# Performance work log

Hardware: AMD Instinct MI355X
Metric: run time of the kernel (lower is better)

Reference implementation:

```python
import jax, jax.numpy as jnp
import numpy as np
import math

B, S, E, H = 2, 2048, 64, 8
N_LAYER = 12
EPS = 1e-5


def setup_inputs() -> dict:
    key = jax.random.key(0)
    ks = jax.random.split(key, 7)
    x = jax.random.normal(ks[0], (B, S, E), dtype=jnp.float32)
    ln_w = jnp.ones((E,), dtype=jnp.float32)
    W_q = 0.02 * jax.random.normal(ks[1], (H, E, E), dtype=jnp.float32)
    W_k = 0.02 * jax.random.normal(ks[2], (H, E, E), dtype=jnp.float32)
    W_v = 0.02 * jax.random.normal(ks[3], (H, E, E), dtype=jnp.float32)
    W_o = (0.02 / math.sqrt(2 * N_LAYER)) * jax.random.normal(ks[4], (E, H * E), dtype=jnp.float32)
    gamma = 1.0 + 0.02 * jax.random.normal(ks[5], (H, 1, 1), dtype=jnp.float32)
    return {"x": x, "ln_w": ln_w, "W_q": W_q, "W_k": W_k, "W_v": W_v, "W_o": W_o, "gamma": gamma}


def reference(x, ln_w, W_q, W_k, W_v, W_o, gamma):
    # LayerNorm (bias=False)
    mu = jnp.mean(x, axis=-1, keepdims=True)
    var = jnp.mean((x - mu) ** 2, axis=-1, keepdims=True)
    xn = (x - mu) * jax.lax.rsqrt(var + EPS) * ln_w  # [B,S,E]

    # per-head full-rank projections: x repeated across heads
    Q = jnp.einsum('bse,hef->bhsf', xn, W_q)  # [B,H,S,E]
    K = jnp.einsum('bse,hef->bhsf', xn, W_k)
    V = jnp.einsum('bse,hef->bhsf', xn, W_v)

    # RBF attention scores: exp(-gamma * ||q_i - k_j||^2 / sqrt(E)), causal
    q2 = jnp.sum(Q * Q, axis=-1)[..., :, None]          # [B,H,S,1]
    k2 = jnp.sum(K * K, axis=-1)[..., None, :]          # [B,H,1,S]
    qk = jnp.einsum('bhse,bhte->bhst', Q, K)            # [B,H,S,S]
    sqdist = q2 + k2 - 2.0 * qk
    scores = jnp.exp(-gamma[None] * sqdist / math.sqrt(E))  # gamma broadcast [H,1,1]
    causal = jnp.tril(jnp.ones((S, S), dtype=scores.dtype))
    scores = scores * causal

    out = jnp.einsum('bhst,bhte->bhse', scores, V)       # [B,H,S,E]
    out = out.transpose(0, 2, 1, 3).reshape(B, S, H * E)  # concat heads
    out = out @ W_o.T                                     # [B,S,E]
    return out
```

## Files before the change

kernel.cpp:

```cpp
#include <hip/hip_runtime.h>
#include <math.h>

typedef __attribute__((ext_vector_type(8))) short bf8;
typedef __attribute__((ext_vector_type(4))) short s4v;
typedef __attribute__((ext_vector_type(16))) float f16v;
typedef __attribute__((ext_vector_type(4))) float f4v;
typedef __attribute__((ext_vector_type(4))) int i4v;

constexpr int CS = 2048;
constexpr float EPS = 1e-5f;
constexpr float LOG2E = 1.44269504088896f;

static __device__ inline short f2bf(float x) {
  union { float f; unsigned u; } v; v.f = x;
  unsigned r = (v.u + 0x7FFFu + ((v.u >> 16) & 1u)) >> 16;
  return (short)r;
}
static __device__ inline float bf2f(short u) {
  union { unsigned u; float f; } v;
  v.u = ((unsigned)(unsigned short)u) << 16;
  return v.f;
}
static __device__ inline unsigned cvt_pk_bf16(float lo, float hi) {
  unsigned d;
  asm("v_cvt_pk_bf16_f32 %0, %1, %2" : "=v"(d) : "v"(lo), "v"(hi));
  return d;
}

__global__ __launch_bounds__(256) void k_qkv(const float* __restrict__ x, const float* __restrict__ ln_w,
                                             const float* __restrict__ Wq, const float* __restrict__ Wk,
                                             const float* __restrict__ Wv, const float* __restrict__ gamma,
                                             short* __restrict__ Qf, short* __restrict__ Kf,
                                             short* __restrict__ Vf, float* __restrict__ aqg) {
  __shared__ short WtL[3 * 64 * 72];
  __shared__ short QtL[2 * 32 * 72];
  __shared__ short KtL[2 * 32 * 72];
  __shared__ float q2s[64];
  __shared__ float bks[64];
  int blk = blockIdx.x;
  int bh = blk & 15, st = blk >> 4;
  int b = bh >> 3, h = bh & 7;
  int t = threadIdx.x, wid = t >> 6, lane = t & 63;
  int l31 = lane & 31, g = lane >> 5;
  int sh = wid >> 1, fh = wid & 1;
  int f = fh * 32 + l31;

  {
    int e0 = (t >> 4) * 4, f0 = (t & 15) * 4;
    const float* srcs[3];
    srcs[0] = Wq + h * 4096; srcs[1] = Wk + h * 4096; srcs[2] = Wv + h * 4096;
#pragma unroll
    for (int wsel = 0; wsel < 3; ++wsel) {
      const float* src = srcs[wsel];
      f4v r0 = *(const f4v*)&src[(e0 + 0) * 64 + f0];
      f4v r1 = *(const f4v*)&src[(e0 + 1) * 64 + f0];
      f4v r2 = *(const f4v*)&src[(e0 + 2) * 64 + f0];
      f4v r3 = *(const f4v*)&src[(e0 + 3) * 64 + f0];
      short* dst = &WtL[wsel * 4608];
      s4v c0, c1, c2, c3;
      c0[0] = f2bf(r0.x); c0[1] = f2bf(r1.x); c0[2] = f2bf(r2.x); c0[3] = f2bf(r3.x);
      c1[0] = f2bf(r0.y); c1[1] = f2bf(r1.y); c1[2] = f2bf(r2.y); c1[3] = f2bf(r3.y);
      c2[0] = f2bf(r0.z); c2[1] = f2bf(r1.z); c2[2] = f2bf(r2.z); c2[3] = f2bf(r3.z);
      c3[0] = f2bf(r0.w); c3[1] = f2bf(r1.w); c3[2] = f2bf(r2.w); c3[3] = f2bf(r3.w);
      *(s4v*)&dst[(f0 + 0) * 72 + e0] = c0;
      *(s4v*)&dst[(f0 + 1) * 72 + e0] = c1;
      *(s4v*)&dst[(f0 + 2) * 72 + e0] = c2;
      *(s4v*)&dst[(f0 + 3) * 72 + e0] = c3;
    }
  }

  int row = b * CS + st * 64 + sh * 32 + l31;
  f4v xv[8];
#pragma unroll
  for (int ks = 0; ks < 4; ++ks) {
    xv[2 * ks]     = *(const f4v*)&x[row * 64 + ks * 16 + g * 8];
    xv[2 * ks + 1] = *(const f4v*)&x[row * 64 + ks * 16 + g * 8 + 4];
  }
  float s = 0.f;
#pragma unroll
  for (int m = 0; m < 8; ++m) s += xv[m].x + xv[m].y + xv[m].z + xv[m].w;
  s += __shfl_xor(s, 32, 64);
  float mu = s * (1.f / 64.f);
  float vs = 0.f;
#pragma unroll
  for (int m = 0; m < 8; ++m) {
#pragma unroll
    for (int j = 0; j < 4; ++j) { float d = xv[m][j] - mu; vs += d * d; }
  }
  vs += __shfl_xor(vs, 32, 64);
  float rs = rsqrtf(vs * (1.f / 64.f) + EPS);
  bf8 af[4];
#pragma unroll
  for (int ks = 0; ks < 4; ++ks) {
    f4v lw0 = *(const f4v*)&ln_w[ks * 16 + g * 8];
    f4v lw1 = *(const f4v*)&ln_w[ks * 16 + g * 8 + 4];
#pragma unroll
    for (int j = 0; j < 4; ++j) {
      af[ks][j]     = f2bf((xv[2 * ks][j] - mu) * rs * lw0[j]);
      af[ks][j + 4] = f2bf((xv[2 * ks + 1][j] - mu) * rs * lw1[j]);
    }
  }
  float gh = gamma[h];
  float cgk = -gh * 0.125f * LOG2E;
  float cgq = gh * 0.25f * LOG2E;
  float icgq2 = 1.f / (cgq * cgq);
  __syncthreads();

  f16v cq; for (int i = 0; i < 16; ++i) cq[i] = 0.f;
#pragma unroll
  for (int ks = 0; ks < 4; ++ks) {
    bf8 bw = *(const bf8*)&WtL[0 * 4608 + f * 72 + ks * 16 + g * 8];
    cq = __builtin_amdgcn_mfma_f32_32x32x16_bf16(af[ks], bw, cq, 0, 0, 0);
  }
#pragma unroll
  for (int r = 0; r < 16; ++r) {
    int rl = (r & 3) + 8 * (r >> 2) + 4 * g;
    QtL[(sh * 32 + rl) * 72 + f] = f2bf(cq[r] * cgq);
  }
  f16v ck; for (int i = 0; i < 16; ++i) ck[i] = 0.f;
#pragma unroll
  for (int ks = 0; ks < 4; ++ks) {
    bf8 bw = *(const bf8*)&WtL[1 * 4608 + f * 72 + ks * 16 + g * 8];
    ck = __builtin_amdgcn_mfma_f32_32x32x16_bf16(af[ks], bw, ck, 0, 0, 0);
  }
#pragma unroll
  for (int r = 0; r < 16; ++r) {
    int rl = (r & 3) + 8 * (r >> 2) + 4 * g;
    KtL[(sh * 32 + rl) * 72 + f] = f2bf(ck[r]);
  }
  f16v cv; for (int i = 0; i < 16; ++i) cv[i] = 0.f;
#pragma unroll
  for (int ks = 0; ks < 4; ++ks) {
    bf8 bw = *(const bf8*)&WtL[2 * 4608 + f * 72 + ks * 16 + g * 8];
    cv = __builtin_amdgcn_mfma_f32_32x32x16_bf16(af[ks], bw, cv, 0, 0, 0);
  }
  __syncthreads();

  {
    int rw = t >> 2, q4 = t & 3;
    float sq = 0.f, sk = 0.f;
#pragma unroll
    for (int m = 0; m < 2; ++m) {
      bf8 vq = *(bf8*)&QtL[rw * 72 + q4 * 16 + m * 8];
      bf8 vk = *(bf8*)&KtL[rw * 72 + q4 * 16 + m * 8];
#pragma unroll
      for (int j = 0; j < 8; ++j) {
        float xq = bf2f(vq[j]); sq += xq * xq;
        float xk = bf2f(vk[j]); sk += xk * xk;
      }
    }
    sq += __shfl_xor(sq, 1, 64); sq += __shfl_xor(sq, 2, 64);
    sk += __shfl_xor(sk, 1, 64); sk += __shfl_xor(sk, 2, 64);
    if (q4 == 0) {
      q2s[rw] = sq * icgq2;
      bks[rw] = exp2f(cgk * sk);
    }
  }
  {
    int ktloc = t >> 7, lm = (t >> 1) & 63, jh = t & 1;
#pragma unroll
    for (int ks = 0; ks < 4; ++ks) {
      int laddr = (ktloc * 32 + (lm & 31)) * 72 + ks * 16 + (lm >> 5) * 8 + jh * 4;
      int gaddr = ((bh * 64 + st * 2 + ktloc) * 4 + ks) * 512 + lm * 8 + jh * 4;
      *(s4v*)&Qf[gaddr] = *(s4v*)&QtL[laddr];
      *(s4v*)&Kf[gaddr] = *(s4v*)&KtL[laddr];
    }
  }
  __syncthreads();

  int kt = st * 2 + sh;
#pragma unroll
  for (int m = 0; m < 4; ++m) {
    s4v pk;
#pragma unroll
    for (int c = 0; c < 4; ++c) {
      int rl = sh * 32 + c + 8 * m + 4 * g;
      pk[c] = f2bf(cv[m * 4 + c] * bks[rl]);
    }
    int addr = ((((bh * 64 + kt) * 2 + fh) * 2 + (m >> 1)) * 64 + (m & 1) * 32 + l31) * 8 + 4 * g;
    *(s4v*)&Vf[addr] = pk;
  }
  if (t < 64) {
    aqg[bh * CS + st * 64 + t] = exp2f(cgk * q2s[t]);
  }
}

__global__ __launch_bounds__(512, 4) void k_attn(const short* __restrict__ Qf, const short* __restrict__ Kf,
                                                 const short* __restrict__ Vf, const float* __restrict__ aqg,
                                                 const float* __restrict__ gamma, short* __restrict__ attnB) {
  __shared__ float red4[4][64][37];
  int bid = blockIdx.x;
  int bh = ((bid & 7) << 1) | ((bid >> 3) & 1);
  int qt = 63 - (bid >> 4);
  int b = bh >> 3, h = bh & 7;
  int t = threadIdx.x, w = t >> 6, lane = t & 63;
  int lam = lane & 31, g = lane >> 5;
  int L = qt + 1;
  int lo = (w * L) >> 3, hi = ((w + 1) * L) >> 3;
  int hiND = hi < qt ? hi : qt;

  bf8 qf[4];
#pragma unroll
  for (int ks = 0; ks < 4; ++ks) qf[ks] = *(const bf8*)&Qf[((bh * 64 + qt) * 4 + ks) * 512 + lane * 8];

  f16v oa0, oa1;
#pragma unroll
  for (int rr = 0; rr < 16; ++rr) { oa0[rr] = 0.f; oa1[rr] = 0.f; }

  const short* kfb = Kf + bh * 131072 + lane * 8;
  const short* vfb = Vf + bh * 131072 + lane * 8;

  for (int kt = lo; kt < hiND; ++kt) {
    const short* kp = kfb + kt * 2048;
    bf8 ak0 = *(const bf8*)(kp);
    bf8 ak1 = *(const bf8*)(kp + 512);
    bf8 ak2 = *(const bf8*)(kp + 1024);
    bf8 ak3 = *(const bf8*)(kp + 1536);

    f16v ct;
#pragma unroll
    for (int rr = 0; rr < 16; ++rr) ct[rr] = 0.f;
    __builtin_amdgcn_s_setprio(1);
    ct = __builtin_amdgcn_mfma_f32_32x32x16_bf16(ak0, qf[0], ct, 0, 0, 0);
    ct = __builtin_amdgcn_mfma_f32_32x32x16_bf16(ak1, qf[1], ct, 0, 0, 0);
    ct = __builtin_amdgcn_mfma_f32_32x32x16_bf16(ak2, qf[2], ct, 0, 0, 0);
    ct = __builtin_amdgcn_mfma_f32_32x32x16_bf16(ak3, qf[3], ct, 0, 0, 0);
    __builtin_amdgcn_s_setprio(0);

    const short* vp = vfb + kt * 2048;
    bf8 av00 = *(const bf8*)(vp);
    bf8 av01 = *(const bf8*)(vp + 512);
    bf8 av10 = *(const bf8*)(vp + 1024);
    bf8 av11 = *(const bf8*)(vp + 1536);

    unsigned pkA[4], pkB[4];
#pragma unroll
    for (int m = 0; m < 4; ++m) {
      float e0 = exp2f(ct[4 * m + 0]);
      float e1 = exp2f(ct[4 * m + 1]);
      float e2 = exp2f(ct[4 * m + 2]);
      float e3 = exp2f(ct[4 * m + 3]);
      pkA[m] = cvt_pk_bf16(e0, e1);
      pkB[m] = cvt_pk_bf16(e2, e3);
    }
    __builtin_amdgcn_s_setprio(1);
#pragma unroll
    for (int ks2 = 0; ks2 < 2; ++ks2) {
      unsigned a0 = pkA[2 * ks2], a1 = pkA[2 * ks2 + 1];
      unsigned b0 = pkB[2 * ks2], b1 = pkB[2 * ks2 + 1];
      asm("v_permlane32_swap_b32 %0, %1" : "+v"(a0), "+v"(a1));
      asm("v_permlane32_swap_b32 %0, %1" : "+v"(b0), "+v"(b1));
      i4v wv;
      wv.x = (int)a0; wv.y = (int)b0; wv.z = (int)a1; wv.w = (int)b1;
      bf8 bs = *(bf8*)&wv;
      oa0 = __builtin_amdgcn_mfma_f32_32x32x16_bf16(ks2 ? av01 : av00, bs, oa0, 0, 0, 0);
      oa1 = __builtin_amdgcn_mfma_f32_32x32x16_bf16(ks2 ? av11 : av10, bs, oa1, 0, 0, 0);
    }
    __builtin_amdgcn_s_setprio(0);
  }

  if (hi > hiND) {
    int kt = qt;
    const short* kp = kfb + kt * 2048;
    bf8 ak0 = *(const bf8*)(kp);
    bf8 ak1 = *(const bf8*)(kp + 512);
    bf8 ak2 = *(const bf8*)(kp + 1024);
    bf8 ak3 = *(const bf8*)(kp + 1536);

    f16v ct;
#pragma unroll
    for (int rr = 0; rr < 16; ++rr) ct[rr] = 0.f;
    ct = __builtin_amdgcn_mfma_f32_32x32x16_bf16(ak0, qf[0], ct, 0, 0, 0);
    ct = __builtin_amdgcn_mfma_f32_32x32x16_bf16(ak1, qf[1], ct, 0, 0, 0);
    ct = __builtin_amdgcn_mfma_f32_32x32x16_bf16(ak2, qf[2], ct, 0, 0, 0);
    ct = __builtin_amdgcn_mfma_f32_32x32x16_bf16(ak3, qf[3], ct, 0, 0, 0);

    const short* vp = vfb + kt * 2048;
    bf8 av00 = *(const bf8*)(vp);
    bf8 av01 = *(const bf8*)(vp + 512);
    bf8 av10 = *(const bf8*)(vp + 1024);
    bf8 av11 = *(const bf8*)(vp + 1536);

    unsigned pkA[4], pkB[4];
#pragma unroll
    for (int m = 0; m < 4; ++m) {
      float sv[4];
#pragma unroll
      for (int ii = 0; ii < 4; ++ii) {
        int kloc = ii + 8 * m + 4 * g;
        float ev = exp2f(ct[4 * m + ii]);
        if (kloc > lam) ev = 0.f;
        sv[ii] = ev;
      }
      pkA[m] = cvt_pk_bf16(sv[0], sv[1]);
      pkB[m] = cvt_pk_bf16(sv[2], sv[3]);
    }
#pragma unroll
    for (int ks2 = 0; ks2 < 2; ++ks2) {
      unsigned a0 = pkA[2 * ks2], a1 = pkA[2 * ks2 + 1];
      unsigned b0 = pkB[2 * ks2], b1 = pkB[2 * ks2 + 1];
      asm("v_permlane32_swap_b32 %0, %1" : "+v"(a0), "+v"(a1));
      asm("v_permlane32_swap_b32 %0, %1" : "+v"(b0), "+v"(b1));
      i4v wv;
      wv.x = (int)a0; wv.y = (int)b0; wv.z = (int)a1; wv.w = (int)b1;
      bf8 bs = *(bf8*)&wv;
      oa0 = __builtin_amdgcn_mfma_f32_32x32x16_bf16(ks2 ? av01 : av00, bs, oa0, 0, 0, 0);
      oa1 = __builtin_amdgcn_mfma_f32_32x32x16_bf16(ks2 ? av11 : av10, bs, oa1, 0, 0, 0);
    }
  }

  if (w < 4) {
#pragma unroll
    for (int rr = 0; rr < 16; ++rr) {
      int e = (rr & 3) + 8 * (rr >> 2) + 4 * g;
      red4[w][e][lam] = oa0[rr];
      red4[w][e + 32][lam] = oa1[rr];
    }
  }
  __syncthreads();
  if (w >= 4) {
#pragma unroll
    for (int rr = 0; rr < 16; ++rr) {
      int e = (rr & 3) + 8 * (rr >> 2) + 4 * g;
      red4[w - 4][e][lam] += oa0[rr];
      red4[w - 4][e + 32][lam] += oa1[rr];
    }
  }
  __syncthreads();
  {
    int q = t >> 4, e0 = (t & 15) * 4;
    float aqv = aqg[bh * CS + qt * 32 + q];
    s4v ov;
#pragma unroll
    for (int jj = 0; jj < 4; ++jj) {
      float v = red4[0][e0 + jj][q] + red4[1][e0 + jj][q] + red4[2][e0 + jj][q] + red4[3][e0 + jj][q];
      ov[jj] = f2bf(v * aqv);
    }
    *(s4v*)&attnB[(b * CS + qt * 32 + q) * 512 + h * 64 + e0] = ov;
  }
}

__global__ __launch_bounds__(256) void k_proj(const short* __restrict__ attnB, const float* __restrict__ Wo,
                                              float* __restrict__ out) {
  __shared__ float red[4][32][36];
  int blk = blockIdx.x, t = threadIdx.x;
  int rt = blk >> 1, fh2 = blk & 1;
  int r0 = rt * 32;
  int kw = t >> 6, lane = t & 63, l31 = lane & 31, g = lane >> 5;
  f16v c; for (int i = 0; i < 16; ++i) c[i] = 0.f;
  int arow = (r0 + l31) * 512;
  int fw = fh2 * 32 + l31;
#pragma unroll
  for (int ks = 0; ks < 8; ++ks) {
    int k0 = kw * 128 + ks * 16 + g * 8;
    bf8 a = *(const bf8*)&attnB[arow + k0];
    f4v w0 = *(const f4v*)&Wo[fw * 512 + k0];
    f4v w1 = *(const f4v*)&Wo[fw * 512 + k0 + 4];
    i4v wp;
    wp.x = (int)cvt_pk_bf16(w0.x, w0.y);
    wp.y = (int)cvt_pk_bf16(w0.z, w0.w);
    wp.z = (int)cvt_pk_bf16(w1.x, w1.y);
    wp.w = (int)cvt_pk_bf16(w1.z, w1.w);
    bf8 bw = *(bf8*)&wp;
    c = __builtin_amdgcn_mfma_f32_32x32x16_bf16(a, bw, c, 0, 0, 0);
  }
#pragma unroll
  for (int rr = 0; rr < 16; ++rr) {
    int rw = (rr & 3) + 8 * (rr >> 2) + 4 * g;
    red[kw][rw][l31] = c[rr];
  }
  __syncthreads();
  {
    int rw = t >> 3, f4 = (t & 7) * 4;
    f4v sum;
#pragma unroll
    for (int j = 0; j < 4; ++j)
      sum[j] = red[0][rw][f4 + j] + red[1][rw][f4 + j] + red[2][rw][f4 + j] + red[3][rw][f4 + j];
    *(f4v*)&out[(r0 + rw) * 64 + fh2 * 32 + f4] = sum;
  }
}

extern "C" void kernel_launch(void* const* d_in, const int* in_sizes, int n_in,
                              void* d_out, int out_size, void* d_ws, size_t ws_size,
                              hipStream_t stream) {
  const float* x     = (const float*)d_in[0];
  const float* ln_w  = (const float*)d_in[1];
  const float* Wq    = (const float*)d_in[2];
  const float* Wk    = (const float*)d_in[3];
  const float* Wv    = (const float*)d_in[4];
  const float* Wo    = (const float*)d_in[5];
  const float* gamma = (const float*)d_in[6];
  float* out = (float*)d_out;

  char* w = (char*)d_ws;
  short* Qf    = (short*)w;
  short* Kf    = (short*)(w + 4194304);
  short* Vf    = (short*)(w + 2 * 4194304);
  float* aqg   = (float*)(w + 3 * 4194304);
  short* attnB = (short*)(w + 3 * 4194304 + 131072);

  hipLaunchKernelGGL(k_qkv,  dim3(512),  dim3(256), 0, stream, x, ln_w, Wq, Wk, Wv, gamma, Qf, Kf, Vf, aqg);
  hipLaunchKernelGGL(k_attn, dim3(1024), dim3(512), 0, stream, Qf, Kf, Vf, aqg, gamma, attnB);
  hipLaunchKernelGGL(k_proj, dim3(256),  dim3(256), 0, stream, attnB, Wo, out);
}
```

Measured before the change: 41.12 us.

## Split attention key range across two blocks and sum partials in projection

Each query tile's causal key range is now split in half across two 256-thread blocks, giving twice as many smaller blocks. Query tiles are interleaved short/long to balance the load. Each half writes its own bf16 partial output buffer, and the output projection runs an extra MFMA per step to add the two partials. Q fragments now come from shared memory instead of registers, which frees registers for higher occupancy. The cost is extra partial-buffer traffic, double bf16 rounding, and more A-operand loads in the projection kernel.

```diff
diff --git a/kernel.cpp b/kernel.cpp
--- a/kernel.cpp
+++ b/kernel.cpp
@@ -185,30 +185,39 @@
   }
 }
 
-__global__ __launch_bounds__(512, 4) void k_attn(const short* __restrict__ Qf, const short* __restrict__ Kf,
+__global__ __launch_bounds__(256, 5) void k_attn(const short* __restrict__ Qf, const short* __restrict__ Kf,
                                                  const short* __restrict__ Vf, const float* __restrict__ aqg,
-                                                 const float* __restrict__ gamma, short* __restrict__ attnB) {
-  __shared__ float red4[4][64][37];
+                                                 const float* __restrict__ gamma,
+                                                 short* __restrict__ P0, short* __restrict__ P1) {
+  __shared__ short QsL[2048];
+  __shared__ float red2[2][64][33];
   int bid = blockIdx.x;
   int bh = ((bid & 7) << 1) | ((bid >> 3) & 1);
-  int qt = 63 - (bid >> 4);
+  int half = (bid >> 4) & 1;
+  int z = bid >> 5;
+  int y = z & 7, j = z >> 3, m = j >> 1;
+  int qt = (j & 1) ? (4 * y + m) : (63 - (4 * y + m));
   int b = bh >> 3, h = bh & 7;
   int t = threadIdx.x, w = t >> 6, lane = t & 63;
   int lam = lane & 31, g = lane >> 5;
   int L = qt + 1;
-  int lo = (w * L) >> 3, hi = ((w + 1) * L) >> 3;
+  int kmid = (qt + 2) >> 1;
+  int k0 = half ? kmid : 0;
+  int k1 = half ? L : kmid;
+  int R = k1 - k0;
+  int lo = k0 + ((w * R) >> 2), hi = k0 + (((w + 1) * R) >> 2);
   int hiND = hi < qt ? hi : qt;
-
-  bf8 qf[4];
-#pragma unroll
-  for (int ks = 0; ks < 4; ++ks) qf[ks] = *(const bf8*)&Qf[((bh * 64 + qt) * 4 + ks) * 512 + lane * 8];
-
+  bool ownDiag = (qt >= lo) && (qt < hi);
+
+  *(bf8*)&QsL[t * 8] = *(const bf8*)&Qf[(bh * 64 + qt) * 2048 + t * 8];
   f16v oa0, oa1;
 #pragma unroll
   for (int rr = 0; rr < 16; ++rr) { oa0[rr] = 0.f; oa1[rr] = 0.f; }
+  __syncthreads();
 
   const short* kfb = Kf + bh * 131072 + lane * 8;
   const short* vfb = Vf + bh * 131072 + lane * 8;
+  int qidx = lane * 8;
 
   for (int kt = lo; kt < hiND; ++kt) {
     const short* kp = kfb + kt * 2048;
@@ -217,14 +226,20 @@
     bf8 ak2 = *(const bf8*)(kp + 1024);
     bf8 ak3 = *(const bf8*)(kp + 1536);
 
+    asm volatile("" : "+v"(qidx));
+    bf8 q0 = *(bf8*)&QsL[qidx];
+    bf8 q1 = *(bf8*)&QsL[qidx + 512];
+    bf8 q2 = *(bf8*)&QsL[qidx + 1024];
+    bf8 q3 = *(bf8*)&QsL[qidx + 1536];
+
     f16v ct;
 #pragma unroll
     for (int rr = 0; rr < 16; ++rr) ct[rr] = 0.f;
     __builtin_amdgcn_s_setprio(1);
-    ct = __builtin_amdgcn_mfma_f32_32x32x16_bf16(ak0, qf[0], ct, 0, 0, 0);
-    ct = __builtin_amdgcn_mfma_f32_32x32x16_bf16(ak1, qf[1], ct, 0, 0, 0);
-    ct = __builtin_amdgcn_mfma_f32_32x32x16_bf16(ak2, qf[2], ct, 0, 0, 0);
-    ct = __builtin_amdgcn_mfma_f32_32x32x16_bf16(ak3, qf[3], ct, 0, 0, 0);
+    ct = __builtin_amdgcn_mfma_f32_32x32x16_bf16(ak0, q0, ct, 0, 0, 0);
+    ct = __builtin_amdgcn_mfma_f32_32x32x16_bf16(ak1, q1, ct, 0, 0, 0);
+    ct = __builtin_amdgcn_mfma_f32_32x32x16_bf16(ak2, q2, ct, 0, 0, 0);
+    ct = __builtin_amdgcn_mfma_f32_32x32x16_bf16(ak3, q3, ct, 0, 0, 0);
     __builtin_amdgcn_s_setprio(0);
 
     const short* vp = vfb + kt * 2048;
@@ -235,13 +250,13 @@
 
     unsigned pkA[4], pkB[4];
 #pragma unroll
-    for (int m = 0; m < 4; ++m) {
-      float e0 = exp2f(ct[4 * m + 0]);
-      float e1 = exp2f(ct[4 * m + 1]);
-      float e2 = exp2f(ct[4 * m + 2]);
-      float e3 = exp2f(ct[4 * m + 3]);
-      pkA[m] = cvt_pk_bf16(e0, e1);
-      pkB[m] = cvt_pk_bf16(e2, e3);
+    for (int mm = 0; mm < 4; ++mm) {
+      float e0 = exp2f(ct[4 * mm + 0]);
+      float e1 = exp2f(ct[4 * mm + 1]);
+      float e2 = exp2f(ct[4 * mm + 2]);
+      float e3 = exp2f(ct[4 * mm + 3]);
+      pkA[mm] = cvt_pk_bf16(e0, e1);
+      pkB[mm] = cvt_pk_bf16(e2, e3);
     }
     __builtin_amdgcn_s_setprio(1);
 #pragma unroll
@@ -259,21 +274,25 @@
     __builtin_amdgcn_s_setprio(0);
   }
 
-  if (hi > hiND) {
+  if (ownDiag) {
     int kt = qt;
     const short* kp = kfb + kt * 2048;
     bf8 ak0 = *(const bf8*)(kp);
     bf8 ak1 = *(const bf8*)(kp + 512);
     bf8 ak2 = *(const bf8*)(kp + 1024);
     bf8 ak3 = *(const bf8*)(kp + 1536);
+    bf8 q0 = *(bf8*)&QsL[qidx];
+    bf8 q1 = *(bf8*)&QsL[qidx + 512];
+    bf8 q2 = *(bf8*)&QsL[qidx + 1024];
+    bf8 q3 = *(bf8*)&QsL[qidx + 1536];
 
     f16v ct;
 #pragma unroll
     for (int rr = 0; rr < 16; ++rr) ct[rr] = 0.f;
-    ct = __builtin_amdgcn_mfma_f32_32x32x16_bf16(ak0, qf[0], ct, 0, 0, 0);
-    ct = __builtin_amdgcn_mfma_f32_32x32x16_bf16(ak1, qf[1], ct, 0, 0, 0);
-    ct = __builtin_amdgcn_mfma_f32_32x32x16_bf16(ak2, qf[2], ct, 0, 0, 0);
-    ct = __builtin_amdgcn_mfma_f32_32x32x16_bf16(ak3, qf[3], ct, 0, 0, 0);
+    ct = __builtin_amdgcn_mfma_f32_32x32x16_bf16(ak0, q0, ct, 0, 0, 0);
+    ct = __builtin_amdgcn_mfma_f32_32x32x16_bf16(ak1, q1, ct, 0, 0, 0);
+    ct = __builtin_amdgcn_mfma_f32_32x32x16_bf16(ak2, q2, ct, 0, 0, 0);
+    ct = __builtin_amdgcn_mfma_f32_32x32x16_bf16(ak3, q3, ct, 0, 0, 0);
 
     const short* vp = vfb + kt * 2048;
     bf8 av00 = *(const bf8*)(vp);
@@ -283,17 +302,17 @@
 
     unsigned pkA[4], pkB[4];
 #pragma unroll
-    for (int m = 0; m < 4; ++m) {
+    for (int mm = 0; mm < 4; ++mm) {
       float sv[4];
 #pragma unroll
       for (int ii = 0; ii < 4; ++ii) {
-        int kloc = ii + 8 * m + 4 * g;
-        float ev = exp2f(ct[4 * m + ii]);
+        int kloc = ii + 8 * mm + 4 * g;
+        float ev = exp2f(ct[4 * mm + ii]);
         if (kloc > lam) ev = 0.f;
         sv[ii] = ev;
       }
-      pkA[m] = cvt_pk_bf16(sv[0], sv[1]);
-      pkB[m] = cvt_pk_bf16(sv[2], sv[3]);
+      pkA[mm] = cvt_pk_bf16(sv[0], sv[1]);
+      pkB[mm] = cvt_pk_bf16(sv[2], sv[3]);
     }
 #pragma unroll
     for (int ks2 = 0; ks2 < 2; ++ks2) {
@@ -309,51 +328,54 @@
     }
   }
 
-  if (w < 4) {
+  if (w < 2) {
 #pragma unroll
     for (int rr = 0; rr < 16; ++rr) {
       int e = (rr & 3) + 8 * (rr >> 2) + 4 * g;
-      red4[w][e][lam] = oa0[rr];
-      red4[w][e + 32][lam] = oa1[rr];
-    }
-  }
-  __syncthreads();
-  if (w >= 4) {
+      red2[w][e][lam] = oa0[rr];
+      red2[w][e + 32][lam] = oa1[rr];
+    }
+  }
+  __syncthreads();
+  if (w >= 2) {
 #pragma unroll
     for (int rr = 0; rr < 16; ++rr) {
       int e = (rr & 3) + 8 * (rr >> 2) + 4 * g;
-      red4[w - 4][e][lam] += oa0[rr];
-      red4[w - 4][e + 32][lam] += oa1[rr];
+      red2[w - 2][e][lam] += oa0[rr];
+      red2[w - 2][e + 32][lam] += oa1[rr];
     }
   }
   __syncthreads();
   {
-    int q = t >> 4, e0 = (t & 15) * 4;
+    short* Ph = half ? P1 : P0;
+    int q = t >> 3, e0 = (t & 7) * 8;
     float aqv = aqg[bh * CS + qt * 32 + q];
-    s4v ov;
-#pragma unroll
-    for (int jj = 0; jj < 4; ++jj) {
-      float v = red4[0][e0 + jj][q] + red4[1][e0 + jj][q] + red4[2][e0 + jj][q] + red4[3][e0 + jj][q];
-      ov[jj] = f2bf(v * aqv);
-    }
-    *(s4v*)&attnB[(b * CS + qt * 32 + q) * 512 + h * 64 + e0] = ov;
-  }
-}
-
-__global__ __launch_bounds__(256) void k_proj(const short* __restrict__ attnB, const float* __restrict__ Wo,
-                                              float* __restrict__ out) {
+    short tmp[8];
+#pragma unroll
+    for (int jj = 0; jj < 8; ++jj)
+      tmp[jj] = f2bf((red2[0][e0 + jj][q] + red2[1][e0 + jj][q]) * aqv);
+    *(bf8*)&Ph[(bh * CS + qt * 32 + q) * 64 + e0] = *(bf8*)&tmp[0];
+  }
+}
+
+__global__ __launch_bounds__(256) void k_proj(const short* __restrict__ P0, const short* __restrict__ P1,
+                                              const float* __restrict__ Wo, float* __restrict__ out) {
   __shared__ float red[4][32][36];
   int blk = blockIdx.x, t = threadIdx.x;
   int rt = blk >> 1, fh2 = blk & 1;
   int r0 = rt * 32;
   int kw = t >> 6, lane = t & 63, l31 = lane & 31, g = lane >> 5;
   f16v c; for (int i = 0; i < 16; ++i) c[i] = 0.f;
-  int arow = (r0 + l31) * 512;
+  int row = r0 + l31;
+  int b = row >> 11, s = row & 2047;
   int fw = fh2 * 32 + l31;
 #pragma unroll
   for (int ks = 0; ks < 8; ++ks) {
     int k0 = kw * 128 + ks * 16 + g * 8;
-    bf8 a = *(const bf8*)&attnB[arow + k0];
+    int h = k0 >> 6, e = k0 & 63;
+    int addr = ((b * 8 + h) * CS + s) * 64 + e;
+    bf8 a0 = *(const bf8*)&P0[addr];
+    bf8 a1 = *(const bf8*)&P1[addr];
     f4v w0 = *(const f4v*)&Wo[fw * 512 + k0];
     f4v w1 = *(const f4v*)&Wo[fw * 512 + k0 + 4];
     i4v wp;
@@ -362,7 +384,8 @@
     wp.z = (int)cvt_pk_bf16(w1.x, w1.y);
     wp.w = (int)cvt_pk_bf16(w1.z, w1.w);
     bf8 bw = *(bf8*)&wp;
-    c = __builtin_amdgcn_mfma_f32_32x32x16_bf16(a, bw, c, 0, 0, 0);
+    c = __builtin_amdgcn_mfma_f32_32x32x16_bf16(a0, bw, c, 0, 0, 0);
+    c = __builtin_amdgcn_mfma_f32_32x32x16_bf16(a1, bw, c, 0, 0, 0);
   }
 #pragma unroll
   for (int rr = 0; rr < 16; ++rr) {
@@ -374,8 +397,8 @@
     int rw = t >> 3, f4 = (t & 7) * 4;
     f4v sum;
 #pragma unroll
-    for (int j = 0; j < 4; ++j)
-      sum[j] = red[0][rw][f4 + j] + red[1][rw][f4 + j] + red[2][rw][f4 + j] + red[3][rw][f4 + j];
+    for (int jj = 0; jj < 4; ++jj)
+      sum[jj] = red[0][rw][f4 + jj] + red[1][rw][f4 + jj] + red[2][rw][f4 + jj] + red[3][rw][f4 + jj];
     *(f4v*)&out[(r0 + rw) * 64 + fh2 * 32 + f4] = sum;
   }
 }
@@ -393,13 +416,14 @@
   float* out = (float*)d_out;
 
   char* w = (char*)d_ws;
-  short* Qf    = (short*)w;
-  short* Kf    = (short*)(w + 4194304);
-  short* Vf    = (short*)(w + 2 * 4194304);
-  float* aqg   = (float*)(w + 3 * 4194304);
-  short* attnB = (short*)(w + 3 * 4194304 + 131072);
+  short* Qf  = (short*)w;
+  short* Kf  = (short*)(w + 4194304);
+  short* Vf  = (short*)(w + 2 * 4194304);
+  float* aqg = (float*)(w + 3 * 4194304);
+  short* P0  = (short*)(w + 3 * 4194304 + 131072);
+  short* P1  = (short*)(w + 4 * 4194304 + 131072);
 
   hipLaunchKernelGGL(k_qkv,  dim3(512),  dim3(256), 0, stream, x, ln_w, Wq, Wk, Wv, gamma, Qf, Kf, Vf, aqg);
-  hipLaunchKernelGGL(k_attn, dim3(1024), dim3(512), 0, stream, Qf, Kf, Vf, aqg, gamma, attnB);
-  hipLaunchKernelGGL(k_proj, dim3(256),  dim3(256), 0, stream, attnB, Wo, out);
-}
+  hipLaunchKernelGGL(k_attn, dim3(2048), dim3(256), 0, stream, Qf, Kf, Vf, aqg, gamma, P0, P1);
+  hipLaunchKernelGGL(k_proj, dim3(256),  dim3(256), 0, stream, P0, P1, Wo, out);
+}
```

Measured after the change: 43.01 us. +4.6%, slower.
